# Performance work log

Hardware: AMD Instinct MI355X
Metric: run time of the kernel (lower is better)

Reference implementation:

```python
import jax, jax.numpy as jnp
import numpy as np

ALPHA = 0.3
N_NODES = 100000
N_EDGES = 640000
D = 128


def setup_inputs() -> dict:
    key = jax.random.key(0)
    k1, k2, k3, k4, k5 = jax.random.split(key, 5)
    return {
        "src_embedding": jax.random.normal(k1, (N_NODES, D), dtype=jnp.float32),
        "dst_embedding": jax.random.normal(k2, (N_NODES, D), dtype=jnp.float32),
        "edge_embedding": jax.random.normal(k3, (N_EDGES, D), dtype=jnp.float32),
        "src_idx": jax.random.randint(k4, (N_EDGES,), 0, N_NODES, dtype=jnp.int64) if jax.config.jax_enable_x64 else jax.random.randint(k4, (N_EDGES,), 0, N_NODES).astype(jnp.int32),
        "dst_idx": jax.random.randint(k5, (N_EDGES,), 0, N_NODES).astype(jnp.int32),
    }


def reference(src_embedding, dst_embedding, edge_embedding, src_idx, dst_idx):
    # msg[e] = src_embedding[src_idx[e]] + edge_embedding[e]   (gather + add)
    msg = src_embedding[src_idx] + edge_embedding              # [E, D]
    # segment mean over destination nodes (DGL mailbox mean reduce)
    agg_sum = jax.ops.segment_sum(msg, dst_idx, num_segments=N_NODES)   # [N, D]
    deg = jax.ops.segment_sum(jnp.ones((msg.shape[0],), msg.dtype), dst_idx,
                              num_segments=N_NODES)            # [N]
    mean = agg_sum / jnp.maximum(deg, 1.0)[:, None]
    out = ALPHA * dst_embedding + (1.0 - ALPHA) * mean
    # DGL: nodes with no incoming messages get zeros for 'agg'
    return jnp.where(deg[:, None] > 0, out, jnp.zeros_like(out))
```

## Files before the change

### kernel.cpp

```cpp
#include <hip/hip_runtime.h>
#include <hip/hip_bf16.h>

#define ALPHA 0.3f
#define D 128
#define STRIDE 40

typedef float v4f __attribute__((ext_vector_type(4)));

__device__ __forceinline__ v4f ldnt4(const float* p) {
    return __builtin_nontemporal_load((const v4f*)p);
}
__device__ __forceinline__ v4f ld4(const float* p) {
    return *(const v4f*)p;
}


__global__ void scatter_kernel(const int* __restrict__ src_idx,
                               const int* __restrict__ dst_idx,
                               int* __restrict__ cursor,
                               int2* __restrict__ perm, int E) {
    int e = blockIdx.x * blockDim.x + threadIdx.x;
    if (e >= E) return;
    int d = dst_idx[e];
    int pos = atomicAdd(&cursor[d], 1);
    perm[(size_t)d * STRIDE + pos] = make_int2(e, src_idx[e]);
}

__global__ void __launch_bounds__(256)
gather_finalize_kernel(const float* __restrict__ src_emb,
                       const float* __restrict__ dst_emb,
                       const float* __restrict__ edge_emb,
                       const int*  __restrict__ cursor,
                       const int2* __restrict__ perm,
                       float* __restrict__ out, int N) {
    int wid = blockIdx.x * (blockDim.x >> 6) + (threadIdx.x >> 6);
    int n = wid * 2 + ((threadIdx.x >> 5) & 1);
    if (n >= N) return;
    int fo = 4 * (threadIdx.x & 31);

    int d = cursor[n];
    const int2* pbase = perm + (size_t)n * STRIDE;

    v4f acc = {0.f, 0.f, 0.f, 0.f};
    int i = 0;
    for (; i + 4 <= d; i += 4) {
        int4 pa = *(const int4*)(pbase + i);
        int4 pb = *(const int4*)(pbase + i + 2);
        v4f e0 = ldnt4(edge_emb + (size_t)pa.x * D + fo);
        v4f s0 = ld4  (src_emb  + (size_t)pa.y * D + fo);
        v4f e1 = ldnt4(edge_emb + (size_t)pa.z * D + fo);
        v4f s1 = ld4  (src_emb  + (size_t)pa.w * D + fo);
        v4f e2 = ldnt4(edge_emb + (size_t)pb.x * D + fo);
        v4f s2 = ld4  (src_emb  + (size_t)pb.y * D + fo);
        v4f e3 = ldnt4(edge_emb + (size_t)pb.z * D + fo);
        v4f s3 = ld4  (src_emb  + (size_t)pb.w * D + fo);
        acc += (e0 + s0) + (e1 + s1) + (e2 + s2) + (e3 + s3);
    }
    for (; i < d; ++i) {
        int2 p = pbase[i];
        v4f ev = ldnt4(edge_emb + (size_t)p.x * D + fo);
        v4f sv = ld4  (src_emb  + (size_t)p.y * D + fo);
        acc += ev + sv;
    }

    v4f o = {0.f, 0.f, 0.f, 0.f};
    if (d > 0) {
        v4f dv = ld4(dst_emb + (size_t)n * D + fo);
        float inv = (1.0f - ALPHA) / (float)d;
        o = ALPHA * dv + acc * inv;
    }
    __builtin_nontemporal_store(o, (v4f*)(out + (size_t)n * D + fo));
}

extern "C" void kernel_launch(void* const* d_in, const int* in_sizes, int n_in,
                              void* d_out, int out_size, void* d_ws, size_t ws_size,
                              hipStream_t stream) {
    const float* src_emb  = (const float*)d_in[0];
    const float* dst_emb  = (const float*)d_in[1];
    const float* edge_emb = (const float*)d_in[2];
    const int*   src_idx  = (const int*)d_in[3];
    const int*   dst_idx  = (const int*)d_in[4];
    float*       out      = (float*)d_out;

    const int N = in_sizes[0] / D;
    const int E = in_sizes[3];

    int2* perm   = (int2*)d_ws;
    int*  cursor = (int*)(perm + (size_t)N * STRIDE);

    hipMemsetAsync(cursor, 0, (size_t)N * sizeof(int), stream);

    int blkE = (E + 255) / 256;
    scatter_kernel<<<blkE, 256, 0, stream>>>(src_idx, dst_idx, cursor, perm, E);

    int grid = (N + 7) / 8;
    gather_finalize_kernel<<<grid, 256, 0, stream>>>(
        src_emb, dst_emb, edge_emb, cursor, perm, out, N);
}
```

Before: 552.2 us.

## Fuse scatter and gather into one persistent kernel with grid barrier

Merges the scatter (bucketing edges by destination) and the gather/finalize kernels into a single persistent kernel sized to full occupancy. A software grid-wide barrier built on an atomic counter separates the two phases, and both phases use grid-stride loops. This removes one kernel launch and the gap between launches. In exchange it adds barrier spin cost, lowers occupancy flexibility, and relies on every block being co-resident or the barrier will deadlock.

```diff
diff --git a/kernel.cpp b/kernel.cpp
--- a/kernel.cpp
+++ b/kernel.cpp
@@ -1,5 +1,4 @@
 #include <hip/hip_runtime.h>
-#include <hip/hip_bf16.h>
 
 #define ALPHA 0.3f
 #define D 128
@@ -15,61 +14,80 @@
 }
 
 
-__global__ void scatter_kernel(const int* __restrict__ src_idx,
-                               const int* __restrict__ dst_idx,
-                               int* __restrict__ cursor,
-                               int2* __restrict__ perm, int E) {
-    int e = blockIdx.x * blockDim.x + threadIdx.x;
-    if (e >= E) return;
-    int d = dst_idx[e];
-    int pos = atomicAdd(&cursor[d], 1);
-    perm[(size_t)d * STRIDE + pos] = make_int2(e, src_idx[e]);
-}
+__global__ void __launch_bounds__(256)
+fused_kernel(const float* __restrict__ src_emb,
+             const float* __restrict__ dst_emb,
+             const float* __restrict__ edge_emb,
+             const int*  __restrict__ src_idx,
+             const int*  __restrict__ dst_idx,
+             int*  cursor,
+             int2* perm,
+             int*  bar,
+             float* __restrict__ out,
+             int N, int E) {
+    const int nblk = gridDim.x;
+    const int tid  = blockIdx.x * 256 + threadIdx.x;
+    const int nthr = nblk * 256;
 
-__global__ void __launch_bounds__(256)
-gather_finalize_kernel(const float* __restrict__ src_emb,
-                       const float* __restrict__ dst_emb,
-                       const float* __restrict__ edge_emb,
-                       const int*  __restrict__ cursor,
-                       const int2* __restrict__ perm,
-                       float* __restrict__ out, int N) {
-    int wid = blockIdx.x * (blockDim.x >> 6) + (threadIdx.x >> 6);
-    int n = wid * 2 + ((threadIdx.x >> 5) & 1);
-    if (n >= N) return;
-    int fo = 4 * (threadIdx.x & 31);
-
-    int d = cursor[n];
-    const int2* pbase = perm + (size_t)n * STRIDE;
-
-    v4f acc = {0.f, 0.f, 0.f, 0.f};
-    int i = 0;
-    for (; i + 4 <= d; i += 4) {
-        int4 pa = *(const int4*)(pbase + i);
-        int4 pb = *(const int4*)(pbase + i + 2);
-        v4f e0 = ldnt4(edge_emb + (size_t)pa.x * D + fo);
-        v4f s0 = ld4  (src_emb  + (size_t)pa.y * D + fo);
-        v4f e1 = ldnt4(edge_emb + (size_t)pa.z * D + fo);
-        v4f s1 = ld4  (src_emb  + (size_t)pa.w * D + fo);
-        v4f e2 = ldnt4(edge_emb + (size_t)pb.x * D + fo);
-        v4f s2 = ld4  (src_emb  + (size_t)pb.y * D + fo);
-        v4f e3 = ldnt4(edge_emb + (size_t)pb.z * D + fo);
-        v4f s3 = ld4  (src_emb  + (size_t)pb.w * D + fo);
-        acc += (e0 + s0) + (e1 + s1) + (e2 + s2) + (e3 + s3);
-    }
-    for (; i < d; ++i) {
-        int2 p = pbase[i];
-        v4f ev = ldnt4(edge_emb + (size_t)p.x * D + fo);
-        v4f sv = ld4  (src_emb  + (size_t)p.y * D + fo);
-        acc += ev + sv;
+    for (int e = tid; e < E; e += nthr) {
+        int d = dst_idx[e];
+        int pos = atomicAdd(&cursor[d], 1);
+        perm[(size_t)d * STRIDE + pos] = make_int2(e, src_idx[e]);
     }
 
-    v4f o = {0.f, 0.f, 0.f, 0.f};
-    if (d > 0) {
-        v4f dv = ld4(dst_emb + (size_t)n * D + fo);
-        float inv = (1.0f - ALPHA) / (float)d;
-        o = ALPHA * dv + acc * inv;
+    __syncthreads();
+    if (threadIdx.x == 0) {
+        __threadfence();
+        __hip_atomic_fetch_add(bar, 1, __ATOMIC_RELAXED, __HIP_MEMORY_SCOPE_AGENT);
+        while (__hip_atomic_load(bar, __ATOMIC_RELAXED, __HIP_MEMORY_SCOPE_AGENT) < nblk)
+            __builtin_amdgcn_s_sleep(2);
+        __threadfence();
     }
-    __builtin_nontemporal_store(o, (v4f*)(out + (size_t)n * D + fo));
+    __syncthreads();
+
+    const int wid0  = blockIdx.x * 4 + (threadIdx.x >> 6);
+    const int nwav  = nblk * 4;
+    const int half  = (threadIdx.x >> 5) & 1;
+    const int fo    = 4 * (threadIdx.x & 31);
+    const int npair = (N + 1) >> 1;
+
+    for (int p = wid0; p < npair; p += nwav) {
+        int n = 2 * p + half;
+        if (n >= N) continue;
+
+        int d = cursor[n];
+        const int2* pbase = perm + (size_t)n * STRIDE;
+
+        v4f acc = {0.f, 0.f, 0.f, 0.f};
+        int i = 0;
+        for (; i + 4 <= d; i += 4) {
+            int4 pa = *(const int4*)(pbase + i);
+            int4 pb = *(const int4*)(pbase + i + 2);
+            v4f e0 = ldnt4(edge_emb + (size_t)pa.x * D + fo);
+            v4f s0 = ld4  (src_emb  + (size_t)pa.y * D + fo);
+            v4f e1 = ldnt4(edge_emb + (size_t)pa.z * D + fo);
+            v4f s1 = ld4  (src_emb  + (size_t)pa.w * D + fo);
+            v4f e2 = ldnt4(edge_emb + (size_t)pb.x * D + fo);
+            v4f s2 = ld4  (src_emb  + (size_t)pb.y * D + fo);
+            v4f e3 = ldnt4(edge_emb + (size_t)pb.z * D + fo);
+            v4f s3 = ld4  (src_emb  + (size_t)pb.w * D + fo);
+            acc += (e0 + s0) + (e1 + s1) + (e2 + s2) + (e3 + s3);
+        }
+        for (; i < d; ++i) {
+            int2 pe = pbase[i];
+            v4f ev = ldnt4(edge_emb + (size_t)pe.x * D + fo);
+            v4f sv = ld4  (src_emb  + (size_t)pe.y * D + fo);
+            acc += ev + sv;
+        }
+
+        v4f o = {0.f, 0.f, 0.f, 0.f};
+        if (d > 0) {
+            v4f dv = ld4(dst_emb + (size_t)n * D + fo);
+            float inv = (1.0f - ALPHA) / (float)d;
+            o = ALPHA * dv + acc * inv;
+        }
+        __builtin_nontemporal_store(o, (v4f*)(out + (size_t)n * D + fo));
+    }
 }
 
 extern "C" void kernel_launch(void* const* d_in, const int* in_sizes, int n_in,
@@ -87,13 +105,25 @@
 
     int2* perm   = (int2*)d_ws;
     int*  cursor = (int*)(perm + (size_t)N * STRIDE);
+    int*  bar    = cursor + N;
 
-    hipMemsetAsync(cursor, 0, (size_t)N * sizeof(int), stream);
+    hipMemsetAsync(cursor, 0, ((size_t)N + 1) * sizeof(int), stream);
 
-    int blkE = (E + 255) / 256;
-    scatter_kernel<<<blkE, 256, 0, stream>>>(src_idx, dst_idx, cursor, perm, E);
+    static int nblk = -1;
+    if (nblk < 0) {
+        int maxB = 0;
+        hipError_t err = hipOccupancyMaxActiveBlocksPerMultiprocessor(
+            &maxB, fused_kernel, 256, 0);
+        if (err != hipSuccess || maxB < 1) maxB = 1;
+        int ncu = 256;
+        hipDeviceProp_t prop;
+        if (hipGetDeviceProperties(&prop, 0) == hipSuccess && prop.multiProcessorCount > 0)
+            ncu = prop.multiProcessorCount;
+        nblk = maxB * ncu;
+        if (nblk > 8192) nblk = 8192;
+    }
 
-    int grid = (N + 7) / 8;
-    gather_finalize_kernel<<<grid, 256, 0, stream>>>(
-        src_emb, dst_emb, edge_emb, cursor, perm, out, N);
+    fused_kernel<<<nblk, 256, 0, stream>>>(
+        src_emb, dst_emb, edge_emb, src_idx, dst_idx,
+        cursor, perm, bar, out, N, E);
 }
```

After: 666.0 us. +20.6%, slower.
